# Kernel optimization log

Hardware: AMD Instinct MI355X
Metric: run time of the kernel (lower is better)

## Reference

```python
import jax, jax.numpy as jnp
import numpy as np

H = 2048   # hidden_dim
E = 8      # num_experts
K = 2      # top_k
N = 4096   # tokens


def setup_inputs() -> dict:
    key = jax.random.key(0)
    ks = jax.random.split(key, 8)
    scale = 0.02
    return {
        "x": jax.random.normal(ks[0], (N, H), dtype=jnp.float32),
        # gate: torch Linear(H, E) -> weight [E, H], bias [E]
        "gate_W": jax.random.normal(ks[1], (E, H), dtype=jnp.float32) * scale,
        "gate_b": jnp.zeros((E,), dtype=jnp.float32),
        # per-expert 2-layer MLP; stored as [E, in, out] for direct einsum
        "W1": jax.random.normal(ks[2], (E, H, H), dtype=jnp.float32) * scale,
        "b1": jnp.zeros((E, H), dtype=jnp.float32),
        "W2": jax.random.normal(ks[3], (E, H, H), dtype=jnp.float32) * scale,
        "b2": jnp.zeros((E, H), dtype=jnp.float32),
    }


def reference(x, gate_W, gate_b, W1, b1, W2, b2):
    # gate softmax over experts: [N, E]
    gate_scores = jax.nn.softmax(x @ gate_W.T + gate_b, axis=-1)
    topk_scores, topk_idx = jax.lax.top_k(gate_scores, K)  # [N, K]
    n = x.shape[0]
    # combine weights: score at selected experts, 0 elsewhere -> [N, E]
    combine = jnp.zeros_like(gate_scores).at[
        jnp.arange(n)[:, None], topk_idx
    ].set(topk_scores)
    # dense per-expert MLP: h [N, E, H]
    h = jax.nn.relu(jnp.einsum('nh,ehf->nef', x, W1) + b1)
    out_e = jnp.einsum('nef,efg->neg', h, W2) + b2  # [N, E, H]
    aggregated = jnp.einsum('ne,neh->nh', combine, out_e)  # [N, H]
    return aggregated, gate_scores
```

## Files before the change

### kernel.cpp

```cpp
#include <hip/hip_runtime.h>
#include <hip/hip_bf16.h>

#define N_TOK 4096
#define HD    2048
#define NE    8

#define BM 128
#define BN 256
#define BK 32
#define NKS (HD/BK)
#define MAXROWS (N_TOK*2 + NE*BM)
#define TMAX (MAXROWS/BM)
#define NNT  (HD/BN)
#define NWG  (TMAX*NNT)
#define TSZ  ((BM+BN)*BK*2)

#define NCOPY 64
#define NCVT  4096
#define NGATE (N_TOK/4)
#define NXCV  (N_TOK*HD/2048)

typedef __attribute__((ext_vector_type(4))) float f32x4;
typedef __attribute__((ext_vector_type(8))) short short8;
typedef __attribute__((ext_vector_type(8))) unsigned short ushort8;

typedef unsigned short u16;
typedef unsigned int   u32;


__device__ __forceinline__ float bf2f(u16 u) {
  union { u32 i; float f; } c; c.i = ((u32)u) << 16; return c.f;
}
__device__ __forceinline__ u16 f2bf(float f) {
  u32 x = __float_as_uint(f);
  u32 r = (x + 0x7fffu + ((x >> 16) & 1u)) >> 16;
  return (u16)r;
}

__device__ __forceinline__ void gload_lds16(const void* gsrc, void* ldst) {
  __builtin_amdgcn_global_load_lds(
      (const __attribute__((address_space(1))) u32*)gsrc,
      (__attribute__((address_space(3))) u32*)ldst, 16, 0, 0);
}

__global__ __launch_bounds__(256) void convert_gate_kernel(
    const float* __restrict__ W1, const float* __restrict__ W2,
    u16* __restrict__ W1T, u16* __restrict__ W2T,
    const float* __restrict__ x, const float* __restrict__ gW,
    const float* __restrict__ gb, float* __restrict__ gate_out,
    int* __restrict__ cnt, int* __restrict__ picks, float* __restrict__ wts,
    u16* __restrict__ Xbf) {
  __shared__ float smem[NE*HD];
  int b = blockIdx.x;
  int t = threadIdx.x;

  if (b >= NCVT + NGATE) {
    size_t base = (size_t)(b - NCVT - NGATE) * 2048 + (size_t)t * 8;
    f32x4 a = *reinterpret_cast<const f32x4*>(x + base);
    f32x4 c = *reinterpret_cast<const f32x4*>(x + base + 4);
    ushort8 v;
    #pragma unroll
    for (int j = 0; j < 4; ++j) { v[j] = f2bf(a[j]); v[4+j] = f2bf(c[j]); }
    *reinterpret_cast<ushort8*>(Xbf + base) = v;
  } else if (b < NCVT) {
    f32x4* tile4 = reinterpret_cast<f32x4*>(smem);
    int bx = b & 7, by = (b >> 3) & 31, z = b >> 8;
    const float* W = (z < NE) ? W1 : W2;
    u16* WT = (z < NE) ? W1T : W2T;
    int e = z & 7;
    size_t ebase = (size_t)e * HD * HD;
    int n0 = bx * 256;
    int k0 = by * 64;
    int l = t & 63, w = t >> 6;
    #pragma unroll
    for (int i = 0; i < 16; ++i) {
      int r = i*4 + w;
      f32x4 v = *reinterpret_cast<const f32x4*>(W + ebase + (size_t)(k0 + r) * HD + n0 + l*4);
      tile4[r*64 + (l ^ ((r >> 3) & 7))] = v;
    }
    __syncthreads();
    #pragma unroll
    for (int i = 0; i < 8; ++i) {
      int np = i*32 + (t >> 3);
      int kc = (t & 7) * 8;
      int c4 = np >> 2, inner = np & 3;
      ushort8 v;
      #pragma unroll
      for (int j = 0; j < 8; ++j) {
        int k = kc + j;
        v[j] = f2bf(smem[(k*64 + (c4 ^ ((k >> 3) & 7)))*4 + inner]);
      }
      *reinterpret_cast<ushort8*>(WT + ebase + (size_t)(n0 + np) * HD + k0 + kc) = v;
    }
  } else {
    float* gwl = smem;
    int gbk = b - NCVT;
    {
      const f32x4* g4 = reinterpret_cast<const f32x4*>(gW);
      f32x4* l4 = reinterpret_cast<f32x4*>(gwl);
      #pragma unroll
      for (int i = 0; i < 16; ++i) l4[i*256 + t] = g4[i*256 + t];
    }
    __syncthreads();
    int wid = (gbk << 2) + (t >> 6);
    int lane = t & 63;
    int copy = gbk & (NCOPY-1);
    const float* xr = x + (size_t)wid * HD;
    float s[NE] = {};
    for (int k = 0; k < HD; k += 256) {
      f32x4 xv = *reinterpret_cast<const f32x4*>(xr + k + lane*4);
      #pragma unroll
      for (int e = 0; e < NE; ++e) {
        f32x4 wv = *reinterpret_cast<const f32x4*>(&gwl[e*HD + k + lane*4]);
        s[e] += xv[0]*wv[0] + xv[1]*wv[1] + xv[2]*wv[2] + xv[3]*wv[3];
      }
    }
    #pragma unroll
    for (int e = 0; e < NE; ++e) {
      float v = s[e];
      #pragma unroll
      for (int off = 32; off > 0; off >>= 1) v += __shfl_xor(v, off);
      s[e] = v + gb[e];
    }
    float mx = s[0];
    #pragma unroll
    for (int e = 1; e < NE; ++e) mx = fmaxf(mx, s[e]);
    float sum = 0.f;
    #pragma unroll
    for (int e = 0; e < NE; ++e) { s[e] = expf(s[e] - mx); sum += s[e]; }
    float inv = 1.f / sum;
    #pragma unroll
    for (int e = 0; e < NE; ++e) s[e] *= inv;
    int e0 = 0; float v0 = s[0];
    #pragma unroll
    for (int e = 1; e < NE; ++e) if (s[e] > v0) { v0 = s[e]; e0 = e; }
    int e1 = -1; float v1 = -1.f;
    #pragma unroll
    for (int e = 0; e < NE; ++e) if (e != e0 && s[e] > v1) { v1 = s[e]; e1 = e; }
    if (lane == 0) {
      #pragma unroll
      for (int e = 0; e < NE; ++e) gate_out[(size_t)wid*NE + e] = s[e];
      int p0 = atomicAdd(&cnt[copy*8 + e0], 1);
      int p1 = atomicAdd(&cnt[copy*8 + e1], 1);
      picks[wid*2]   = (p0 << 9) | (copy << 3) | e0;
      picks[wid*2+1] = (p1 << 9) | (copy << 3) | e1;
      wts[wid*2]   = v0;
      wts[wid*2+1] = v1;
    }
  }
}

__global__ void scan_kernel(int* meta) {
  int e = threadIdx.x;
  if (e < NE) {
    int run = 0;
    for (int c = 0; c < NCOPY; ++c) {
      meta[512 + c*8 + e] = run;
      run += meta[c*8 + e];
    }
    meta[1024 + e] = run;
  }
}

__global__ void fill_kernel(const int* __restrict__ picks, const int* __restrict__ meta,
                            int* __restrict__ slot, int* __restrict__ rowTok) {
  int i = blockIdx.x * 256 + threadIdx.x;
  if (i >= N_TOK*2) return;
  int p = picks[i];
  int e = p & 7, c = (p >> 3) & (NCOPY-1), pos = p >> 9;
  int base = 0;
  #pragma unroll
  for (int ee = 0; ee < NE; ++ee)
    if (ee < e) base += ((meta[1024+ee] + BM - 1) >> 7) << 7;
  int row = base + meta[512 + c*8 + e] + pos;
  slot[i] = row;
  rowTok[row] = i >> 1;
}

__device__ __forceinline__ void compute_ktile(
    const char* ldsA, const char* ldsB, f32x4 (&acc)[4][4],
    int wr, int wc, int l15, int lhi) {
  short8 af[4], bfr[4];
  #pragma unroll
  for (int m = 0; m < 4; ++m) {
    int r = wr*64 + m*16 + l15;
    int c = lhi ^ ((r >> 1) & 3);
    af[m] = *reinterpret_cast<const short8*>(ldsA + r*64 + c*16);
  }
  #pragma unroll
  for (int n = 0; n < 4; ++n) {
    int r = wc*64 + n*16 + l15;
    int c = lhi ^ ((r >> 1) & 3);
    bfr[n] = *reinterpret_cast<const short8*>(ldsB + r*64 + c*16);
  }
  #pragma unroll
  for (int m = 0; m < 4; ++m)
    #pragma unroll
    for (int n = 0; n < 4; ++n)
      acc[m][n] = __builtin_amdgcn_mfma_f32_16x16x32_bf16(af[m], bfr[n], acc[m][n], 0, 0, 0);
}

template<bool RELU, bool IND>
__global__ __launch_bounds__(512, 4) void moe_gemm_kernel(
    const u16* __restrict__ A,
    const u16* __restrict__ WT,
    const float* __restrict__ bias,
    u16* __restrict__ Out,
    const int* __restrict__ tot,
    const int* __restrict__ rowTok) {
  int bid = blockIdx.x;
  int wg = (bid & 7) * (NWG/8) + (bid >> 3);
  int t  = wg >> 3;
  int nt = wg & 7;
  int tiles = 0, rows = 0, e = 0, tstart = 0, rbase = 0;
  #pragma unroll
  for (int i = 0; i < NE; ++i) {
    int tl = (tot[i] + BM - 1) >> 7;
    if (t >= tiles && t < tiles + tl) { e = i; tstart = tiles; rbase = rows; }
    tiles += tl; rows += tl << 7;
  }
  if (t >= tiles) return;
  int rowBase = rbase + (t - tstart) * BM;

  const u16* Bp = WT + ((size_t)e * HD + (size_t)nt * BN) * HD;

  __shared__ char lds[3*TSZ];

  int tid = threadIdx.x;
  int lane = tid & 63;
  int wv = tid >> 6;
  int wr = wv >> 2, wc = wv & 3;
  int l15 = lane & 15, lhi = lane >> 4;

  int aR = tid >> 2;
  int aC = (tid & 3) ^ ((aR >> 1) & 3);
  const u16* Asrc;
  if (IND) {
    int tk = rowTok[rowBase + aR];
    if (tk < 0) tk = 0;
    Asrc = A + (size_t)tk * HD + aC*8;
  } else {
    Asrc = A + (size_t)(rowBase + aR) * HD + aC*8;
  }
  int b1R = 128 + aR;
  int b1C = (tid & 3) ^ ((b1R >> 1) & 3);
  const u16* Bsrc0 = Bp + (size_t)aR * HD + aC*8;
  const u16* Bsrc1 = Bp + (size_t)b1R * HD + b1C*8;
  int ldsAoff = tid*16;
  int ldsB0off = BM*BK*2 + tid*16;
  int ldsB1off = BM*BK*2 + (512 + tid)*16;

  f32x4 acc[4][4] = {};

  gload_lds16(Asrc,       lds + ldsAoff);
  gload_lds16(Bsrc0,      lds + ldsB0off);
  gload_lds16(Bsrc1,      lds + ldsB1off);
  gload_lds16(Asrc  + BK, lds + TSZ + ldsAoff);
  gload_lds16(Bsrc0 + BK, lds + TSZ + ldsB0off);
  gload_lds16(Bsrc1 + BK, lds + TSZ + ldsB1off);

  int rd = 0;
  for (int ks = 0; ks < NKS - 2; ++ks) {
    asm volatile("s_waitcnt vmcnt(3)" ::: "memory");
    __builtin_amdgcn_s_barrier();
    int wi = rd + 2; if (wi >= 3) wi -= 3;
    int koff = (ks+2)*BK;
    gload_lds16(Asrc  + koff, lds + wi*TSZ + ldsAoff);
    gload_lds16(Bsrc0 + koff, lds + wi*TSZ + ldsB0off);
    gload_lds16(Bsrc1 + koff, lds + wi*TSZ + ldsB1off);
    __builtin_amdgcn_sched_barrier(0);
    compute_ktile(lds + rd*TSZ, lds + rd*TSZ + BM*BK*2, acc, wr, wc, l15, lhi);
    if (++rd == 3) rd = 0;
  }
  asm volatile("s_waitcnt vmcnt(3)" ::: "memory");
  __builtin_amdgcn_s_barrier();
  compute_ktile(lds + rd*TSZ, lds + rd*TSZ + BM*BK*2, acc, wr, wc, l15, lhi);
  if (++rd == 3) rd = 0;
  asm volatile("s_waitcnt vmcnt(0)" ::: "memory");
  __builtin_amdgcn_s_barrier();
  compute_ktile(lds + rd*TSZ, lds + rd*TSZ + BM*BK*2, acc, wr, wc, l15, lhi);

  int orow = rowBase + wr*64;
  int ocol = nt*BN + wc*64;
  const float* bp = bias + (size_t)e * HD + ocol;
  #pragma unroll
  for (int n = 0; n < 4; ++n) {
    float bv = bp[n*16 + l15];
    #pragma unroll
    for (int m = 0; m < 4; ++m) {
      #pragma unroll
      for (int j = 0; j < 4; ++j) {
        float v = acc[m][n][j] + bv;
        if (RELU) v = fmaxf(v, 0.f);
        Out[(size_t)(orow + m*16 + lhi*4 + j) * HD + (ocol + n*16 + l15)] = f2bf(v);
      }
    }
  }
}

__global__ __launch_bounds__(256) void combine_kernel(
    const u16* __restrict__ Y, const int* __restrict__ slot,
    const float* __restrict__ wts, float* __restrict__ out) {
  int n = blockIdx.x;
  int r0 = slot[n*2], r1 = slot[n*2+1];
  float w0 = wts[n*2], w1 = wts[n*2+1];
  int c = threadIdx.x * 8;
  ushort8 y0 = *reinterpret_cast<const ushort8*>(Y + (size_t)r0*HD + c);
  ushort8 y1 = *reinterpret_cast<const ushort8*>(Y + (size_t)r1*HD + c);
  f32x4 o0, o1;
  #pragma unroll
  for (int j = 0; j < 4; ++j) {
    o0[j] = w0*bf2f(y0[j])   + w1*bf2f(y1[j]);
    o1[j] = w0*bf2f(y0[4+j]) + w1*bf2f(y1[4+j]);
  }
  f32x4* dst = reinterpret_cast<f32x4*>(out + (size_t)n*HD + c);
  dst[0] = o0; dst[1] = o1;
}

extern "C" void kernel_launch(void* const* d_in, const int* in_sizes, int n_in,
                              void* d_out, int out_size, void* d_ws, size_t ws_size,
                              hipStream_t stream) {
  const float* x     = (const float*)d_in[0];
  const float* gateW = (const float*)d_in[1];
  const float* gateb = (const float*)d_in[2];
  const float* W1    = (const float*)d_in[3];
  const float* b1    = (const float*)d_in[4];
  const float* W2    = (const float*)d_in[5];
  const float* b2    = (const float*)d_in[6];
  float* out      = (float*)d_out;
  float* gate_out = out + (size_t)N_TOK * HD;

  char* ws = (char*)d_ws;
  size_t o = 0;
  u16* W1T = (u16*)(ws + o); o += (size_t)NE*HD*HD*2;
  u16* W2T = (u16*)(ws + o); o += (size_t)NE*HD*HD*2;
  u16* Xbf = (u16*)(ws + o);
  u16* Y   = Xbf;
  o += (size_t)MAXROWS*HD*2;
  u16* Hbuf = (u16*)(ws + o); o += (size_t)MAXROWS*HD*2;
  int*   meta   = (int*)(ws + o);   o += 8192;
  int*   picks  = (int*)(ws + o);   o += (size_t)N_TOK*2*4;
  float* wts    = (float*)(ws + o); o += (size_t)N_TOK*2*4;
  int*   slot   = (int*)(ws + o);   o += (size_t)N_TOK*2*4;
  int*   rowTok = (int*)(ws + o);   o += (size_t)MAXROWS*4;

  hipMemsetAsync(meta, 0, NCOPY*8*4, stream);
  hipMemsetAsync(rowTok, 0xFF, (size_t)MAXROWS*4, stream);

  convert_gate_kernel<<<dim3(NCVT + NGATE + NXCV), 256, 0, stream>>>(
      W1, W2, W1T, W2T, x, gateW, gateb, gate_out, meta, picks, wts, Xbf);
  scan_kernel<<<1, 64, 0, stream>>>(meta);
  fill_kernel<<<(N_TOK*2)/256, 256, 0, stream>>>(picks, meta, slot, rowTok);
  moe_gemm_kernel<true,  true ><<<dim3(NWG), 512, 0, stream>>>(Xbf,  W1T, b1, Hbuf,
                                                               meta + 1024, rowTok);
  moe_gemm_kernel<false, false><<<dim3(NWG), 512, 0, stream>>>(Hbuf, W2T, b2, Y,
                                                               meta + 1024, rowTok);
  combine_kernel<<<N_TOK, 256, 0, stream>>>(Y, slot, wts, out);
}
```

Before: 304.4 us.

## Move W2 conversion into the first GEMM launch to overlap with compute

The W2 fp32-to-bf16 transpose conversion leaves the initial convert/gate kernel and runs as extra workgroups appended to the first expert GEMM launch. The bandwidth-bound conversion can then overlap with the compute-bound GEMM1 tiles, and the first kernel gets shorter. The combined kernel shares the LDS declaration between both roles. Conversion blocks appended after the GEMM blocks may run late and compete with GEMM tiles for CUs.

```diff
diff --git a/kernel.cpp b/kernel.cpp
--- a/kernel.cpp
+++ b/kernel.cpp
@@ -16,9 +16,10 @@
 #define TSZ  ((BM+BN)*BK*2)
 
 #define NCOPY 64
-#define NCVT  4096
+#define NCVT1 2048
 #define NGATE (N_TOK/4)
 #define NXCV  (N_TOK*HD/2048)
+#define NCVT2 2048
 
 typedef __attribute__((ext_vector_type(4))) float f32x4;
 typedef __attribute__((ext_vector_type(8))) short short8;
@@ -44,8 +45,7 @@
 }
 
 __global__ __launch_bounds__(256) void convert_gate_kernel(
-    const float* __restrict__ W1, const float* __restrict__ W2,
-    u16* __restrict__ W1T, u16* __restrict__ W2T,
+    const float* __restrict__ W1, u16* __restrict__ W1T,
     const float* __restrict__ x, const float* __restrict__ gW,
     const float* __restrict__ gb, float* __restrict__ gate_out,
     int* __restrict__ cnt, int* __restrict__ picks, float* __restrict__ wts,
@@ -54,20 +54,17 @@
   int b = blockIdx.x;
   int t = threadIdx.x;
 
-  if (b >= NCVT + NGATE) {
-    size_t base = (size_t)(b - NCVT - NGATE) * 2048 + (size_t)t * 8;
+  if (b >= NCVT1 + NGATE) {
+    size_t base = (size_t)(b - NCVT1 - NGATE) * 2048 + (size_t)t * 8;
     f32x4 a = *reinterpret_cast<const f32x4*>(x + base);
     f32x4 c = *reinterpret_cast<const f32x4*>(x + base + 4);
     ushort8 v;
     #pragma unroll
     for (int j = 0; j < 4; ++j) { v[j] = f2bf(a[j]); v[4+j] = f2bf(c[j]); }
     *reinterpret_cast<ushort8*>(Xbf + base) = v;
-  } else if (b < NCVT) {
+  } else if (b < NCVT1) {
     f32x4* tile4 = reinterpret_cast<f32x4*>(smem);
-    int bx = b & 7, by = (b >> 3) & 31, z = b >> 8;
-    const float* W = (z < NE) ? W1 : W2;
-    u16* WT = (z < NE) ? W1T : W2T;
-    int e = z & 7;
+    int bx = b & 7, by = (b >> 3) & 31, e = b >> 8;
     size_t ebase = (size_t)e * HD * HD;
     int n0 = bx * 256;
     int k0 = by * 64;
@@ -75,7 +72,7 @@
     #pragma unroll
     for (int i = 0; i < 16; ++i) {
       int r = i*4 + w;
-      f32x4 v = *reinterpret_cast<const f32x4*>(W + ebase + (size_t)(k0 + r) * HD + n0 + l*4);
+      f32x4 v = *reinterpret_cast<const f32x4*>(W1 + ebase + (size_t)(k0 + r) * HD + n0 + l*4);
       tile4[r*64 + (l ^ ((r >> 3) & 7))] = v;
     }
     __syncthreads();
@@ -90,11 +87,11 @@
         int k = kc + j;
         v[j] = f2bf(smem[(k*64 + (c4 ^ ((k >> 3) & 7)))*4 + inner]);
       }
-      *reinterpret_cast<ushort8*>(WT + ebase + (size_t)(n0 + np) * HD + k0 + kc) = v;
+      *reinterpret_cast<ushort8*>(W1T + ebase + (size_t)(n0 + np) * HD + k0 + kc) = v;
     }
   } else {
     float* gwl = smem;
-    int gbk = b - NCVT;
+    int gbk = b - NCVT1;
     {
       const f32x4* g4 = reinterpret_cast<const f32x4*>(gW);
       f32x4* l4 = reinterpret_cast<f32x4*>(gwl);
@@ -201,14 +198,11 @@
 }
 
 template<bool RELU, bool IND>
-__global__ __launch_bounds__(512, 4) void moe_gemm_kernel(
-    const u16* __restrict__ A,
-    const u16* __restrict__ WT,
-    const float* __restrict__ bias,
-    u16* __restrict__ Out,
-    const int* __restrict__ tot,
-    const int* __restrict__ rowTok) {
-  int bid = blockIdx.x;
+__device__ __forceinline__ void gemm_role(
+    char* lds, int bid,
+    const u16* __restrict__ A, const u16* __restrict__ WT,
+    const float* __restrict__ bias, u16* __restrict__ Out,
+    const int* __restrict__ tot, const int* __restrict__ rowTok) {
   int wg = (bid & 7) * (NWG/8) + (bid >> 3);
   int t  = wg >> 3;
   int nt = wg & 7;
@@ -223,8 +217,6 @@
   int rowBase = rbase + (t - tstart) * BM;
 
   const u16* Bp = WT + ((size_t)e * HD + (size_t)nt * BN) * HD;
-
-  __shared__ char lds[3*TSZ];
 
   int tid = threadIdx.x;
   int lane = tid & 63;
@@ -296,6 +288,57 @@
       }
     }
   }
+}
+
+__global__ __launch_bounds__(512, 4) void gemm1_convw2_kernel(
+    const u16* __restrict__ A, const u16* __restrict__ WT,
+    const float* __restrict__ bias, u16* __restrict__ Out,
+    const int* __restrict__ tot, const int* __restrict__ rowTok,
+    const float* __restrict__ W2, u16* __restrict__ W2T) {
+  __shared__ char lds[3*TSZ];
+  int bid = blockIdx.x;
+  if (bid < NWG) {
+    gemm_role<true, true>(lds, bid, A, WT, bias, Out, tot, rowTok);
+  } else {
+    float* smem = reinterpret_cast<float*>(lds);
+    f32x4* tile4 = reinterpret_cast<f32x4*>(lds);
+    int b2 = bid - NWG;
+    int bx = b2 & 7, by = (b2 >> 3) & 31, e = b2 >> 8;
+    size_t ebase = (size_t)e * HD * HD;
+    int n0 = bx * 256;
+    int k0 = by * 64;
+    int t = threadIdx.x;
+    int l = t & 63, w = t >> 6;
+    #pragma unroll
+    for (int i = 0; i < 8; ++i) {
+      int r = i*8 + w;
+      f32x4 v = *reinterpret_cast<const f32x4*>(W2 + ebase + (size_t)(k0 + r) * HD + n0 + l*4);
+      tile4[r*64 + (l ^ ((r >> 3) & 7))] = v;
+    }
+    __syncthreads();
+    #pragma unroll
+    for (int i = 0; i < 4; ++i) {
+      int np = i*64 + (t >> 3);
+      int kc = (t & 7) * 8;
+      int c4 = np >> 2, inner = np & 3;
+      ushort8 v;
+      #pragma unroll
+      for (int j = 0; j < 8; ++j) {
+        int k = kc + j;
+        v[j] = f2bf(smem[(k*64 + (c4 ^ ((k >> 3) & 7)))*4 + inner]);
+      }
+      *reinterpret_cast<ushort8*>(W2T + ebase + (size_t)(n0 + np) * HD + k0 + kc) = v;
+    }
+  }
+}
+
+template<bool RELU, bool IND>
+__global__ __launch_bounds__(512, 4) void moe_gemm_kernel(
+    const u16* __restrict__ A, const u16* __restrict__ WT,
+    const float* __restrict__ bias, u16* __restrict__ Out,
+    const int* __restrict__ tot, const int* __restrict__ rowTok) {
+  __shared__ char lds[3*TSZ];
+  gemm_role<RELU, IND>(lds, blockIdx.x, A, WT, bias, Out, tot, rowTok);
 }
 
 __global__ __launch_bounds__(256) void combine_kernel(
@@ -347,12 +390,12 @@
   hipMemsetAsync(meta, 0, NCOPY*8*4, stream);
   hipMemsetAsync(rowTok, 0xFF, (size_t)MAXROWS*4, stream);
 
-  convert_gate_kernel<<<dim3(NCVT + NGATE + NXCV), 256, 0, stream>>>(
-      W1, W2, W1T, W2T, x, gateW, gateb, gate_out, meta, picks, wts, Xbf);
+  convert_gate_kernel<<<dim3(NCVT1 + NGATE + NXCV), 256, 0, stream>>>(
+      W1, W1T, x, gateW, gateb, gate_out, meta, picks, wts, Xbf);
   scan_kernel<<<1, 64, 0, stream>>>(meta);
   fill_kernel<<<(N_TOK*2)/256, 256, 0, stream>>>(picks, meta, slot, rowTok);
-  moe_gemm_kernel<true,  true ><<<dim3(NWG), 512, 0, stream>>>(Xbf,  W1T, b1, Hbuf,
-                                                               meta + 1024, rowTok);
+  gemm1_convw2_kernel<<<dim3(NWG + NCVT2), 512, 0, stream>>>(
+      Xbf, W1T, b1, Hbuf, meta + 1024, rowTok, W2, W2T);
   moe_gemm_kernel<false, false><<<dim3(NWG), 512, 0, stream>>>(Hbuf, W2T, b2, Y,
                                                                meta + 1024, rowTok);
   combine_kernel<<<N_TOK, 256, 0, stream>>>(Y, slot, wts, out);
```

After: 292.9 us (median of 2 runs). 1.04x faster.
